# Optimization experiments

Measured on AMD Instinct MI355X. Metric: run time of the kernel, lower is better.

Reference implementation:

```python
import jax, jax.numpy as jnp
import numpy as np

B, L, H, S = 8, 2048, 8, 128


def setup_inputs() -> dict:
    key = jax.random.key(0)
    k1, k2, k3 = jax.random.split(key, 3)
    x = jax.random.normal(k1, (B, L, S), dtype=jnp.float32)
    W = jax.random.normal(k2, (L, H), dtype=jnp.float32)          # per-head Toeplitz logits, W[j, h] fills diagonal -j
    A = jax.random.normal(k3, (H * S, H * S), dtype=jnp.float32)  # bilinear form for stage-2 attention
    return {"x": x, "W": W, "A": A}


def reference(x, W, A):
    Bb, Ll, Ss = x.shape
    Hh = W.shape[1]
    HS = Hh * Ss
    # Stage 1: causal Toeplitz softmax attention per head.
    # Original fills diagonal -j of W_h with W[j, h], masks strictly-upper with -inf, softmaxes rows.
    d = jnp.arange(Ll)[:, None] - jnp.arange(Ll)[None, :]          # (L, L), i - j
    logits = jnp.where(d[..., None] >= 0,
                       W[jnp.clip(d, 0, Ll - 1)],                  # (L, L, H), W[i-j, h] on valid band
                       -jnp.inf)
    P = jax.nn.softmax(logits, axis=1)                             # softmax over key axis j
    attn = jnp.einsum('ijh,bjs->bihs', P, x).reshape(Bb, Ll, HS)   # heads concatenated
    X1 = jnp.concatenate([attn, x], axis=-1)                       # (B, L, (H+1)*S)
    # Stage 2: single-query bilinear attention from last token over previous tokens.
    q = X1[:, -1, :HS]                                             # (B, HS)
    keys = X1[:, :-1, :HS]                                         # (B, L-1, HS)
    scores = jnp.einsum('bd,de,ble->bl', q, A, keys)               # (B, L-1)
    w2 = jax.nn.softmax(scores, axis=-1)
    # values are the raw-x slice X1[:, :-1, HS:] == x[:, :-1, :]
    out = jnp.einsum('bl,bls->bs', w2, x[:, :-1, :])               # (B, S)
    return out
```

## Files before the change

kernel.cpp:

```cpp
#include <hip/hip_runtime.h>

#define L 2048
#define H 8
#define S 128
#define B 8
#define HS 1024

__global__ __launch_bounds__(256) void kA_prep_qpart(const float* __restrict__ W,
                                                     const float* __restrict__ x,
                                                     float* __restrict__ E,
                                                     float* __restrict__ Z,
                                                     float* __restrict__ partial_q,
                                                     unsigned* __restrict__ counters) {
  const int b = blockIdx.x, jc = blockIdx.y;
  const int t = threadIdx.x;
  if (b == 0 && jc == 0 && t == 0) counters[0] = 0u;

  __shared__ float ew[128][H];
  __shared__ float part[8][H][S];
  __shared__ float tot[256];

  const int base = jc * 128;
  const int dhi = L - 1 - base;
#pragma unroll
  for (int k = 0; k < 4; ++k) {
    const int idx = t + k * 256;
    const int i = idx >> 3, h = idx & 7;
    ew[i][h] = expf(W[(size_t)(dhi - i) * H + h]);
  }

  if (b == 0 && jc < H) {
    const int h = jc;
    const int d0 = t * 8;
    float e[8];
    float run = 0.f;
#pragma unroll
    for (int k = 0; k < 8; ++k) {
      float v = expf(W[(size_t)(d0 + k) * H + h]);
      e[k] = v; run += v;
    }
    tot[t] = run;
    __syncthreads();
    for (int off = 1; off < 256; off <<= 1) {
      float v = (t >= off) ? tot[t - off] : 0.f;
      __syncthreads();
      tot[t] += v;
      __syncthreads();
    }
    float c = (t == 0) ? 0.f : tot[t - 1];
#pragma unroll
    for (int k = 0; k < 8; ++k) {
      c += e[k];
      E[h * L + d0 + k] = e[k];
      Z[h * L + d0 + k] = c;
    }
  }
  __syncthreads();

  const int s4 = t & 31;
  const int r = t >> 5;
  const float4* __restrict__ x4 = (const float4*)(x + (size_t)b * L * S);
  float4 acc[H];
#pragma unroll
  for (int h = 0; h < H; ++h) acc[h] = make_float4(0.f, 0.f, 0.f, 0.f);
#pragma unroll
  for (int k = 0; k < 16; ++k) {
    const int ll = k * 8 + r;
    const int l = base + ll;
    const float4 xv = x4[(size_t)l * 32 + s4];
#pragma unroll
    for (int h = 0; h < H; ++h) {
      const float w = ew[ll][h];
      acc[h].x += w * xv.x; acc[h].y += w * xv.y;
      acc[h].z += w * xv.z; acc[h].w += w * xv.w;
    }
  }
#pragma unroll
  for (int h = 0; h < H; ++h) {
    part[r][h][s4 * 4 + 0] = acc[h].x;
    part[r][h][s4 * 4 + 1] = acc[h].y;
    part[r][h][s4 * 4 + 2] = acc[h].z;
    part[r][h][s4 * 4 + 3] = acc[h].w;
  }
  __syncthreads();
#pragma unroll
  for (int k = 0; k < 4; ++k) {
    const int idx = t + k * 256;
    const int h = idx >> 7, s = idx & 127;
    float sm = 0.f;
#pragma unroll
    for (int rr = 0; rr < 8; ++rr) sm += part[rr][h][s];
    partial_q[((size_t)b * 16 + jc) * HS + idx] = sm;
  }
}

__global__ __launch_bounds__(256) void kB_v(const float* __restrict__ partial_q,
                                            const float* __restrict__ Z,
                                            const float* __restrict__ A,
                                            float* __restrict__ partial_v) {
  const int ebase = blockIdx.x * 128;
  const int dc = blockIdx.y;
  const int dbase = dc * 64;
  const int t = threadIdx.x;
  __shared__ float ql[8][64];
  __shared__ float p2[2][8][128];
  const float invZ = 1.f / Z[(dc >> 1) * L + (L - 1)];
#pragma unroll
  for (int k = 0; k < 2; ++k) {
    const int o = t + k * 256;
    const int bb = o >> 6, dl = o & 63;
    const float* __restrict__ pq = partial_q + ((size_t)bb * 16) * HS + dbase + dl;
    float a0 = 0.f, a1 = 0.f, a2 = 0.f, a3 = 0.f;
#pragma unroll
    for (int j4 = 0; j4 < 16; j4 += 4) {
      a0 += pq[(size_t)(j4 + 0) * HS];
      a1 += pq[(size_t)(j4 + 1) * HS];
      a2 += pq[(size_t)(j4 + 2) * HS];
      a3 += pq[(size_t)(j4 + 3) * HS];
    }
    ql[bb][dl] = ((a0 + a1) + (a2 + a3)) * invZ;
  }
  __syncthreads();
  const int el = t & 127, dg = t >> 7;
  const int e = ebase + el;
  const float* __restrict__ Ab = A + (size_t)(dbase + dg * 32) * HS + e;
  float acc[8] = {0.f, 0.f, 0.f, 0.f, 0.f, 0.f, 0.f, 0.f};
#pragma unroll 4
  for (int dd = 0; dd < 32; ++dd) {
    const float a = Ab[(size_t)dd * HS];
    const int d = dg * 32 + dd;
    acc[0] += ql[0][d] * a;
    acc[1] += ql[1][d] * a;
    acc[2] += ql[2][d] * a;
    acc[3] += ql[3][d] * a;
    acc[4] += ql[4][d] * a;
    acc[5] += ql[5][d] * a;
    acc[6] += ql[6][d] * a;
    acc[7] += ql[7][d] * a;
  }
#pragma unroll
  for (int bb = 0; bb < 8; ++bb) p2[dg][bb][el] = acc[bb];
  __syncthreads();
#pragma unroll
  for (int k = 0; k < 4; ++k) {
    const int idx = t + k * 256;
    const int bb = idx >> 7, el2 = idx & 127;
    partial_v[((size_t)bb * 16 + dc) * HS + ebase + el2] = p2[0][bb][el2] + p2[1][bb][el2];
  }
}

__global__ __launch_bounds__(256) void kC_u(const float* __restrict__ x,
                                            const float* __restrict__ partial_v,
                                            float* __restrict__ u_pad) {
  const int b = blockIdx.x, jc = blockIdx.y;
  const int t = threadIdx.x;
  __shared__ float vs[HS];
  __shared__ float up[2][H][128];
#pragma unroll
  for (int k = 0; k < 4; ++k) {
    const int i = t + k * 256;
    float a = 0.f;
#pragma unroll
    for (int dcc = 0; dcc < 16; ++dcc) a += partial_v[((size_t)b * 16 + dcc) * HS + i];
    vs[i] = a;
  }
  __syncthreads();
  const int jl = t & 127, sq = t >> 7;
  const int j = jc * 128 + jl;
  const float4* __restrict__ xr = (const float4*)(x + ((size_t)b * L + j) * S) + sq * 16;
  float4 xv[16];
#pragma unroll
  for (int i = 0; i < 16; ++i) xv[i] = xr[i];
  float acc[H];
#pragma unroll
  for (int h = 0; h < H; ++h) {
    const float4* __restrict__ vv = (const float4*)(vs + h * S + sq * 64);
    float a = 0.f;
#pragma unroll
    for (int i = 0; i < 16; ++i) {
      const float4 w = vv[i];
      a += xv[i].x * w.x + xv[i].y * w.y + xv[i].z * w.z + xv[i].w * w.w;
    }
    acc[h] = a;
  }
#pragma unroll
  for (int h = 0; h < H; ++h) up[sq][h][jl] = acc[h];
  __syncthreads();
#pragma unroll
  for (int k = 0; k < 4; ++k) {
    const int idx = t + k * 256;
    const int h = idx >> 7, j2 = idx & 127;
    const float sv = up[0][h][j2] + up[1][h][j2];
    const size_t rowbase = (size_t)(b * H + h) * (2 * L);
    u_pad[rowbase + jc * 128 + j2] = 0.f;
    u_pad[rowbase + L + jc * 128 + j2] = sv;
  }
}

__global__ __launch_bounds__(256) void kD_conv(const float* __restrict__ u_pad,
                                               const float* __restrict__ E,
                                               const float* __restrict__ Z,
                                               float* __restrict__ partial_s) {
  const int job = blockIdx.x;
  const int b = job / 72;
  const int rr = job - b * 72;
  int lt = 0, c = 0;
  while (c + (lt / 2 + 1) <= rr) { c += lt / 2 + 1; ++lt; }
  const int dtt = rr - c;
  const int l0 = lt * 128;
  const int dbase = dtt * 256;
  const int t = threadIdx.x;
  const int tsub = t & 31;
  const int h = t >> 5;
  const int Lb = l0 + tsub * 4;
  const float* __restrict__ ur = u_pad + (size_t)(b * H + h) * (2 * L) + L;
  const float4* __restrict__ Eh4 = (const float4*)(E + h * L);
  float acc0 = 0.f, acc1 = 0.f, acc2 = 0.f, acc3 = 0.f;
  float4 lo = *(const float4*)(ur + Lb - dbase - 4);
  float4 hi = *(const float4*)(ur + Lb - dbase);
#pragma unroll 4
  for (int dd = 0; dd < 256; dd += 4) {
    const int d0 = dbase + dd;
    float4 ev  = Eh4[d0 >> 2];
    float4 nlo = *(const float4*)(ur + Lb - d0 - 8);
    acc0 += ev.x * hi.x; acc1 += ev.x * hi.y; acc2 += ev.x * hi.z; acc3 += ev.x * hi.w;
    acc0 += ev.y * lo.w; acc1 += ev.y * hi.x; acc2 += ev.y * hi.y; acc3 += ev.y * hi.z;
    acc0 += ev.z * lo.z; acc1 += ev.z * lo.w; acc2 += ev.z * hi.x; acc3 += ev.z * hi.y;
    acc0 += ev.w * lo.y; acc1 += ev.w * lo.z; acc2 += ev.w * lo.w; acc3 += ev.w * hi.x;
    hi = lo; lo = nlo;
  }
  __shared__ float sred[H][128];
  const float4 zv = *(const float4*)&Z[h * L + Lb];
  sred[h][tsub * 4 + 0] = acc0 / zv.x;
  sred[h][tsub * 4 + 1] = acc1 / zv.y;
  sred[h][tsub * 4 + 2] = acc2 / zv.z;
  sred[h][tsub * 4 + 3] = acc3 / zv.w;
  __syncthreads();
  if (t < 128) {
    float sc = 0.f;
#pragma unroll
    for (int hh = 0; hh < H; ++hh) sc += sred[hh][t];
    partial_s[((size_t)b * 8 + dtt) * L + l0 + t] = sc;
  }
}

__global__ __launch_bounds__(256) void kF_out(const float* __restrict__ x,
                                              const float* __restrict__ partial_s,
                                              float* __restrict__ partial,
                                              unsigned* __restrict__ counters,
                                              float* __restrict__ out) {
  const int b = blockIdx.x, c = blockIdx.y;
  const int t = threadIdx.x;
  __shared__ float ep[L];
  __shared__ float red[256];
  __shared__ float part[8][S];

  const int l0 = t * 8;
  const int ltq = t >> 5;
  float sc[8];
#pragma unroll
  for (int k = 0; k < 8; ++k) sc[k] = 0.f;
  for (int dtt = 0; dtt <= ltq; ++dtt) {
    const float4* __restrict__ ps = (const float4*)(partial_s + ((size_t)b * 8 + dtt) * L + l0);
    const float4 a = ps[0], c4 = ps[1];
    sc[0] += a.x;  sc[1] += a.y;  sc[2] += a.z;  sc[3] += a.w;
    sc[4] += c4.x; sc[5] += c4.y; sc[6] += c4.z; sc[7] += c4.w;
  }
  if (t == 255) sc[7] = -3.4e38f;
  float mx = sc[0];
#pragma unroll
  for (int k = 1; k < 8; ++k) mx = fmaxf(mx, sc[k]);
  red[t] = mx;
  __syncthreads();
  for (int off = 128; off > 0; off >>= 1) {
    if (t < off) red[t] = fmaxf(red[t], red[t + off]);
    __syncthreads();
  }
  mx = red[0];
  __syncthreads();
  float e[8];
  float sm = 0.f;
#pragma unroll
  for (int k = 0; k < 8; ++k) {
    e[k] = (l0 + k < L - 1) ? expf(sc[k] - mx) : 0.f;
    sm += e[k];
  }
  red[t] = sm;
  __syncthreads();
  for (int off = 128; off > 0; off >>= 1) {
    if (t < off) red[t] += red[t + off];
    __syncthreads();
  }
  const float inv = 1.f / red[0];
#pragma unroll
  for (int k = 0; k < 8; ++k) ep[l0 + k] = e[k] * inv;
  __syncthreads();

  const int s4 = t & 31;
  const int r = t >> 5;
  const int base = c * 128;
  const float4* __restrict__ x4 = (const float4*)(x + (size_t)b * L * S);
  float4 acc = make_float4(0.f, 0.f, 0.f, 0.f);
#pragma unroll
  for (int k = 0; k < 16; ++k) {
    const int l = base + k * 8 + r;
    const float w = ep[l];
    const float4 xv = x4[(size_t)l * 32 + s4];
    acc.x += w * xv.x; acc.y += w * xv.y; acc.z += w * xv.z; acc.w += w * xv.w;
  }
  part[r][s4 * 4 + 0] = acc.x;
  part[r][s4 * 4 + 1] = acc.y;
  part[r][s4 * 4 + 2] = acc.z;
  part[r][s4 * 4 + 3] = acc.w;
  __syncthreads();
  if (t < S) {
    float smv = 0.f;
#pragma unroll
    for (int rr = 0; rr < 8; ++rr) smv += part[rr][t];
    partial[((size_t)b * 16 + c) * S + t] = smv;
  }
  __threadfence();
  __syncthreads();
  __shared__ unsigned lastFlag;
  if (t == 0)
    lastFlag = (atomicAdd(&counters[0], 1u) == (unsigned)(B * 16 - 1)) ? 1u : 0u;
  __syncthreads();
  if (lastFlag) {
#pragma unroll
    for (int k = 0; k < 4; ++k) {
      const int idx = t + k * 256;
      const int b2 = idx >> 7, s = idx & 127;
      float a = 0.f;
#pragma unroll 4
      for (int cc = 0; cc < 16; ++cc) a += partial[((size_t)b2 * 16 + cc) * S + s];
      out[b2 * S + s] = a;
    }
  }
}

extern "C" void kernel_launch(void* const* d_in, const int* in_sizes, int n_in,
                              void* d_out, int out_size, void* d_ws, size_t ws_size,
                              hipStream_t stream) {
  const float* x = (const float*)d_in[0];
  const float* W = (const float*)d_in[1];
  const float* A = (const float*)d_in[2];
  float* out = (float*)d_out;

  float* ws        = (float*)d_ws;
  float* E         = ws;
  float* Z         = E + H * L;
  float* partial_q = Z + H * L;
  float* partial_v = partial_q + (size_t)B * 16 * HS;
  float* u_pad     = partial_v + (size_t)B * 16 * HS;
  float* partial_s = u_pad + (size_t)B * H * 2 * L;
  float* partial   = partial_s + (size_t)B * 8 * L;
  unsigned* counters = (unsigned*)(partial + (size_t)B * 16 * S);

  kA_prep_qpart<<<dim3(B, 16), 256, 0, stream>>>(W, x, E, Z, partial_q, counters);
  kB_v         <<<dim3(8, 16), 256, 0, stream>>>(partial_q, Z, A, partial_v);
  kC_u         <<<dim3(B, 16), 256, 0, stream>>>(x, partial_v, u_pad);
  kD_conv      <<<B * 72,      256, 0, stream>>>(u_pad, E, Z, partial_s);
  kF_out       <<<dim3(B, 16), 256, 0, stream>>>(x, partial_s, partial, counters, out);
}
```

Before: 58.83 us.

## Double block size to 512 threads across all five kernels, halving per-thread work

Every kernel now launches 512 threads per block with the same grid, so each thread handles half as many rows, d-slices or lags, and shared-memory partial buffers and reductions grow to match. The aim is more waves in flight per block, which hides memory latency on grids that are small (128 blocks for most kernels). In exchange the shared-memory reductions get longer and more syncs are spent per block. Some loops also gain split accumulators.

```diff
diff --git a/kernel.cpp b/kernel.cpp
--- a/kernel.cpp
+++ b/kernel.cpp
@@ -6,7 +6,7 @@
 #define B 8
 #define HS 1024
 
-__global__ __launch_bounds__(256) void kA_prep_qpart(const float* __restrict__ W,
+__global__ __launch_bounds__(512) void kA_prep_qpart(const float* __restrict__ W,
                                                      const float* __restrict__ x,
                                                      float* __restrict__ E,
                                                      float* __restrict__ Z,
@@ -17,31 +17,31 @@
   if (b == 0 && jc == 0 && t == 0) counters[0] = 0u;
 
   __shared__ float ew[128][H];
-  __shared__ float part[8][H][S];
-  __shared__ float tot[256];
+  __shared__ float part[16][H][S];
+  __shared__ float tot[512];
 
   const int base = jc * 128;
   const int dhi = L - 1 - base;
 #pragma unroll
-  for (int k = 0; k < 4; ++k) {
-    const int idx = t + k * 256;
+  for (int k = 0; k < 2; ++k) {
+    const int idx = t + k * 512;
     const int i = idx >> 3, h = idx & 7;
     ew[i][h] = expf(W[(size_t)(dhi - i) * H + h]);
   }
 
   if (b == 0 && jc < H) {
     const int h = jc;
-    const int d0 = t * 8;
-    float e[8];
+    const int d0 = t * 4;
+    float e[4];
     float run = 0.f;
 #pragma unroll
-    for (int k = 0; k < 8; ++k) {
+    for (int k = 0; k < 4; ++k) {
       float v = expf(W[(size_t)(d0 + k) * H + h]);
       e[k] = v; run += v;
     }
     tot[t] = run;
     __syncthreads();
-    for (int off = 1; off < 256; off <<= 1) {
+    for (int off = 1; off < 512; off <<= 1) {
       float v = (t >= off) ? tot[t - off] : 0.f;
       __syncthreads();
       tot[t] += v;
@@ -49,7 +49,7 @@
     }
     float c = (t == 0) ? 0.f : tot[t - 1];
 #pragma unroll
-    for (int k = 0; k < 8; ++k) {
+    for (int k = 0; k < 4; ++k) {
       c += e[k];
       E[h * L + d0 + k] = e[k];
       Z[h * L + d0 + k] = c;
@@ -64,8 +64,8 @@
 #pragma unroll
   for (int h = 0; h < H; ++h) acc[h] = make_float4(0.f, 0.f, 0.f, 0.f);
 #pragma unroll
-  for (int k = 0; k < 16; ++k) {
-    const int ll = k * 8 + r;
+  for (int k = 0; k < 8; ++k) {
+    const int ll = k * 16 + r;
     const int l = base + ll;
     const float4 xv = x4[(size_t)l * 32 + s4];
 #pragma unroll
@@ -84,17 +84,17 @@
   }
   __syncthreads();
 #pragma unroll
-  for (int k = 0; k < 4; ++k) {
-    const int idx = t + k * 256;
+  for (int k = 0; k < 2; ++k) {
+    const int idx = t + k * 512;
     const int h = idx >> 7, s = idx & 127;
     float sm = 0.f;
 #pragma unroll
-    for (int rr = 0; rr < 8; ++rr) sm += part[rr][h][s];
+    for (int rr = 0; rr < 16; ++rr) sm += part[rr][h][s];
     partial_q[((size_t)b * 16 + jc) * HS + idx] = sm;
   }
 }
 
-__global__ __launch_bounds__(256) void kB_v(const float* __restrict__ partial_q,
+__global__ __launch_bounds__(512) void kB_v(const float* __restrict__ partial_q,
                                             const float* __restrict__ Z,
                                             const float* __restrict__ A,
                                             float* __restrict__ partial_v) {
@@ -103,12 +103,10 @@
   const int dbase = dc * 64;
   const int t = threadIdx.x;
   __shared__ float ql[8][64];
-  __shared__ float p2[2][8][128];
+  __shared__ float p2[4][8][128];
   const float invZ = 1.f / Z[(dc >> 1) * L + (L - 1)];
-#pragma unroll
-  for (int k = 0; k < 2; ++k) {
-    const int o = t + k * 256;
-    const int bb = o >> 6, dl = o & 63;
+  {
+    const int bb = t >> 6, dl = t & 63;
     const float* __restrict__ pq = partial_q + ((size_t)bb * 16) * HS + dbase + dl;
     float a0 = 0.f, a1 = 0.f, a2 = 0.f, a3 = 0.f;
 #pragma unroll
@@ -123,12 +121,12 @@
   __syncthreads();
   const int el = t & 127, dg = t >> 7;
   const int e = ebase + el;
-  const float* __restrict__ Ab = A + (size_t)(dbase + dg * 32) * HS + e;
+  const float* __restrict__ Ab = A + (size_t)(dbase + dg * 16) * HS + e;
   float acc[8] = {0.f, 0.f, 0.f, 0.f, 0.f, 0.f, 0.f, 0.f};
 #pragma unroll 4
-  for (int dd = 0; dd < 32; ++dd) {
+  for (int dd = 0; dd < 16; ++dd) {
     const float a = Ab[(size_t)dd * HS];
-    const int d = dg * 32 + dd;
+    const int d = dg * 16 + dd;
     acc[0] += ql[0][d] * a;
     acc[1] += ql[1][d] * a;
     acc[2] += ql[2][d] * a;
@@ -142,42 +140,48 @@
   for (int bb = 0; bb < 8; ++bb) p2[dg][bb][el] = acc[bb];
   __syncthreads();
 #pragma unroll
-  for (int k = 0; k < 4; ++k) {
-    const int idx = t + k * 256;
+  for (int k = 0; k < 2; ++k) {
+    const int idx = t + k * 512;
     const int bb = idx >> 7, el2 = idx & 127;
-    partial_v[((size_t)bb * 16 + dc) * HS + ebase + el2] = p2[0][bb][el2] + p2[1][bb][el2];
-  }
-}
-
-__global__ __launch_bounds__(256) void kC_u(const float* __restrict__ x,
+    partial_v[((size_t)bb * 16 + dc) * HS + ebase + el2] =
+        (p2[0][bb][el2] + p2[1][bb][el2]) + (p2[2][bb][el2] + p2[3][bb][el2]);
+  }
+}
+
+__global__ __launch_bounds__(512) void kC_u(const float* __restrict__ x,
                                             const float* __restrict__ partial_v,
                                             float* __restrict__ u_pad) {
   const int b = blockIdx.x, jc = blockIdx.y;
   const int t = threadIdx.x;
   __shared__ float vs[HS];
-  __shared__ float up[2][H][128];
-#pragma unroll
-  for (int k = 0; k < 4; ++k) {
-    const int i = t + k * 256;
-    float a = 0.f;
-#pragma unroll
-    for (int dcc = 0; dcc < 16; ++dcc) a += partial_v[((size_t)b * 16 + dcc) * HS + i];
-    vs[i] = a;
+  __shared__ float up[4][H][128];
+#pragma unroll
+  for (int k = 0; k < 2; ++k) {
+    const int i = t + k * 512;
+    float a0 = 0.f, a1 = 0.f, a2 = 0.f, a3 = 0.f;
+#pragma unroll
+    for (int dcc = 0; dcc < 16; dcc += 4) {
+      a0 += partial_v[((size_t)b * 16 + dcc + 0) * HS + i];
+      a1 += partial_v[((size_t)b * 16 + dcc + 1) * HS + i];
+      a2 += partial_v[((size_t)b * 16 + dcc + 2) * HS + i];
+      a3 += partial_v[((size_t)b * 16 + dcc + 3) * HS + i];
+    }
+    vs[i] = (a0 + a1) + (a2 + a3);
   }
   __syncthreads();
   const int jl = t & 127, sq = t >> 7;
   const int j = jc * 128 + jl;
-  const float4* __restrict__ xr = (const float4*)(x + ((size_t)b * L + j) * S) + sq * 16;
-  float4 xv[16];
-#pragma unroll
-  for (int i = 0; i < 16; ++i) xv[i] = xr[i];
+  const float4* __restrict__ xr = (const float4*)(x + ((size_t)b * L + j) * S) + sq * 8;
+  float4 xv[8];
+#pragma unroll
+  for (int i = 0; i < 8; ++i) xv[i] = xr[i];
   float acc[H];
 #pragma unroll
   for (int h = 0; h < H; ++h) {
-    const float4* __restrict__ vv = (const float4*)(vs + h * S + sq * 64);
+    const float4* __restrict__ vv = (const float4*)(vs + h * S + sq * 32);
     float a = 0.f;
 #pragma unroll
-    for (int i = 0; i < 16; ++i) {
+    for (int i = 0; i < 8; ++i) {
       const float4 w = vv[i];
       a += xv[i].x * w.x + xv[i].y * w.y + xv[i].z * w.z + xv[i].w * w.w;
     }
@@ -187,17 +191,17 @@
   for (int h = 0; h < H; ++h) up[sq][h][jl] = acc[h];
   __syncthreads();
 #pragma unroll
-  for (int k = 0; k < 4; ++k) {
-    const int idx = t + k * 256;
+  for (int k = 0; k < 2; ++k) {
+    const int idx = t + k * 512;
     const int h = idx >> 7, j2 = idx & 127;
-    const float sv = up[0][h][j2] + up[1][h][j2];
+    const float sv = (up[0][h][j2] + up[1][h][j2]) + (up[2][h][j2] + up[3][h][j2]);
     const size_t rowbase = (size_t)(b * H + h) * (2 * L);
     u_pad[rowbase + jc * 128 + j2] = 0.f;
     u_pad[rowbase + L + jc * 128 + j2] = sv;
   }
 }
 
-__global__ __launch_bounds__(256) void kD_conv(const float* __restrict__ u_pad,
+__global__ __launch_bounds__(512) void kD_conv(const float* __restrict__ u_pad,
                                                const float* __restrict__ E,
                                                const float* __restrict__ Z,
                                                float* __restrict__ partial_s) {
@@ -208,10 +212,11 @@
   while (c + (lt / 2 + 1) <= rr) { c += lt / 2 + 1; ++lt; }
   const int dtt = rr - c;
   const int l0 = lt * 128;
-  const int dbase = dtt * 256;
   const int t = threadIdx.x;
   const int tsub = t & 31;
-  const int h = t >> 5;
+  const int h = (t >> 5) & 7;
+  const int dh = t >> 8;
+  const int dbase = dtt * 256 + dh * 128;
   const int Lb = l0 + tsub * 4;
   const float* __restrict__ ur = u_pad + (size_t)(b * H + h) * (2 * L) + L;
   const float4* __restrict__ Eh4 = (const float4*)(E + h * L);
@@ -219,7 +224,7 @@
   float4 lo = *(const float4*)(ur + Lb - dbase - 4);
   float4 hi = *(const float4*)(ur + Lb - dbase);
 #pragma unroll 4
-  for (int dd = 0; dd < 256; dd += 4) {
+  for (int dd = 0; dd < 128; dd += 4) {
     const int d0 = dbase + dd;
     float4 ev  = Eh4[d0 >> 2];
     float4 nlo = *(const float4*)(ur + Lb - d0 - 8);
@@ -229,22 +234,22 @@
     acc0 += ev.w * lo.y; acc1 += ev.w * lo.z; acc2 += ev.w * lo.w; acc3 += ev.w * hi.x;
     hi = lo; lo = nlo;
   }
-  __shared__ float sred[H][128];
+  __shared__ float sred[2][H][128];
   const float4 zv = *(const float4*)&Z[h * L + Lb];
-  sred[h][tsub * 4 + 0] = acc0 / zv.x;
-  sred[h][tsub * 4 + 1] = acc1 / zv.y;
-  sred[h][tsub * 4 + 2] = acc2 / zv.z;
-  sred[h][tsub * 4 + 3] = acc3 / zv.w;
+  sred[dh][h][tsub * 4 + 0] = acc0 / zv.x;
+  sred[dh][h][tsub * 4 + 1] = acc1 / zv.y;
+  sred[dh][h][tsub * 4 + 2] = acc2 / zv.z;
+  sred[dh][h][tsub * 4 + 3] = acc3 / zv.w;
   __syncthreads();
   if (t < 128) {
     float sc = 0.f;
 #pragma unroll
-    for (int hh = 0; hh < H; ++hh) sc += sred[hh][t];
+    for (int hh = 0; hh < H; ++hh) sc += sred[0][hh][t] + sred[1][hh][t];
     partial_s[((size_t)b * 8 + dtt) * L + l0 + t] = sc;
   }
 }
 
-__global__ __launch_bounds__(256) void kF_out(const float* __restrict__ x,
+__global__ __launch_bounds__(512) void kF_out(const float* __restrict__ x,
                                               const float* __restrict__ partial_s,
                                               float* __restrict__ partial,
                                               unsigned* __restrict__ counters,
@@ -252,48 +257,42 @@
   const int b = blockIdx.x, c = blockIdx.y;
   const int t = threadIdx.x;
   __shared__ float ep[L];
-  __shared__ float red[256];
-  __shared__ float part[8][S];
-
-  const int l0 = t * 8;
-  const int ltq = t >> 5;
-  float sc[8];
-#pragma unroll
-  for (int k = 0; k < 8; ++k) sc[k] = 0.f;
+  __shared__ float red[512];
+  __shared__ float part[16][S];
+
+  const int l0 = t * 4;
+  const int ltq = t >> 6;
+  float sc[4] = {0.f, 0.f, 0.f, 0.f};
   for (int dtt = 0; dtt <= ltq; ++dtt) {
-    const float4* __restrict__ ps = (const float4*)(partial_s + ((size_t)b * 8 + dtt) * L + l0);
-    const float4 a = ps[0], c4 = ps[1];
-    sc[0] += a.x;  sc[1] += a.y;  sc[2] += a.z;  sc[3] += a.w;
-    sc[4] += c4.x; sc[5] += c4.y; sc[6] += c4.z; sc[7] += c4.w;
-  }
-  if (t == 255) sc[7] = -3.4e38f;
-  float mx = sc[0];
-#pragma unroll
-  for (int k = 1; k < 8; ++k) mx = fmaxf(mx, sc[k]);
+    const float4 a = *(const float4*)(partial_s + ((size_t)b * 8 + dtt) * L + l0);
+    sc[0] += a.x; sc[1] += a.y; sc[2] += a.z; sc[3] += a.w;
+  }
+  if (t == 511) sc[3] = -3.4e38f;
+  float mx = fmaxf(fmaxf(sc[0], sc[1]), fmaxf(sc[2], sc[3]));
   red[t] = mx;
   __syncthreads();
-  for (int off = 128; off > 0; off >>= 1) {
+  for (int off = 256; off > 0; off >>= 1) {
     if (t < off) red[t] = fmaxf(red[t], red[t + off]);
     __syncthreads();
   }
   mx = red[0];
   __syncthreads();
-  float e[8];
+  float e[4];
   float sm = 0.f;
 #pragma unroll
-  for (int k = 0; k < 8; ++k) {
+  for (int k = 0; k < 4; ++k) {
     e[k] = (l0 + k < L - 1) ? expf(sc[k] - mx) : 0.f;
     sm += e[k];
   }
   red[t] = sm;
   __syncthreads();
-  for (int off = 128; off > 0; off >>= 1) {
+  for (int off = 256; off > 0; off >>= 1) {
     if (t < off) red[t] += red[t + off];
     __syncthreads();
   }
   const float inv = 1.f / red[0];
 #pragma unroll
-  for (int k = 0; k < 8; ++k) ep[l0 + k] = e[k] * inv;
+  for (int k = 0; k < 4; ++k) ep[l0 + k] = e[k] * inv;
   __syncthreads();
 
   const int s4 = t & 31;
@@ -302,8 +301,8 @@
   const float4* __restrict__ x4 = (const float4*)(x + (size_t)b * L * S);
   float4 acc = make_float4(0.f, 0.f, 0.f, 0.f);
 #pragma unroll
-  for (int k = 0; k < 16; ++k) {
-    const int l = base + k * 8 + r;
+  for (int k = 0; k < 8; ++k) {
+    const int l = base + k * 16 + r;
     const float w = ep[l];
     const float4 xv = x4[(size_t)l * 32 + s4];
     acc.x += w * xv.x; acc.y += w * xv.y; acc.z += w * xv.z; acc.w += w * xv.w;
@@ -316,7 +315,7 @@
   if (t < S) {
     float smv = 0.f;
 #pragma unroll
-    for (int rr = 0; rr < 8; ++rr) smv += part[rr][t];
+    for (int rr = 0; rr < 16; ++rr) smv += part[rr][t];
     partial[((size_t)b * 16 + c) * S + t] = smv;
   }
   __threadfence();
@@ -327,8 +326,8 @@
   __syncthreads();
   if (lastFlag) {
 #pragma unroll
-    for (int k = 0; k < 4; ++k) {
-      const int idx = t + k * 256;
+    for (int k = 0; k < 2; ++k) {
+      const int idx = t + k * 512;
       const int b2 = idx >> 7, s = idx & 127;
       float a = 0.f;
 #pragma unroll 4
@@ -356,9 +355,9 @@
   float* partial   = partial_s + (size_t)B * 8 * L;
   unsigned* counters = (unsigned*)(partial + (size_t)B * 16 * S);
 
-  kA_prep_qpart<<<dim3(B, 16), 256, 0, stream>>>(W, x, E, Z, partial_q, counters);
-  kB_v         <<<dim3(8, 16), 256, 0, stream>>>(partial_q, Z, A, partial_v);
-  kC_u         <<<dim3(B, 16), 256, 0, stream>>>(x, partial_v, u_pad);
-  kD_conv      <<<B * 72,      256, 0, stream>>>(u_pad, E, Z, partial_s);
-  kF_out       <<<dim3(B, 16), 256, 0, stream>>>(x, partial_s, partial, counters, out);
-}
+  kA_prep_qpart<<<dim3(B, 16), 512, 0, stream>>>(W, x, E, Z, partial_q, counters);
+  kB_v         <<<dim3(8, 16), 512, 0, stream>>>(partial_q, Z, A, partial_v);
+  kC_u         <<<dim3(B, 16), 512, 0, stream>>>(x, partial_v, u_pad);
+  kD_conv      <<<B * 72,      512, 0, stream>>>(u_pad, E, Z, partial_s);
+  kF_out       <<<dim3(B, 16), 512, 0, stream>>>(x, partial_s, partial, counters, out);
+}
```

Result: no change. 58.81 us (-0.0%).
